# Kernel optimization log

Hardware: AMD Instinct MI355X
Metric: run time of the kernel (lower is better)

Reference implementation:

```python
import jax, jax.numpy as jnp
import numpy as np

S = 8192      # sequence length
D = 768       # bert_out_dim
NA = 256      # num aspects
NO = 256      # num opinions
MAXW = 40     # max span width (width_embedding has 40 entries)
NCAT = 13
NPOL = 3


def setup_inputs() -> dict:
    key = jax.random.key(0)
    ks = jax.random.split(key, 9)
    word_rep = jax.random.normal(ks[0], (S, D), jnp.float32)
    a_head = jax.random.randint(ks[1], (NA,), 0, S - MAXW)
    a_w = jax.random.randint(ks[2], (NA,), 1, MAXW + 1)
    aspects = jnp.stack([a_head, a_head + a_w], axis=-1)  # [NA,2] (head,tail), head<tail
    o_head = jax.random.randint(ks[3], (NO,), 0, S - MAXW)
    o_w = jax.random.randint(ks[4], (NO,), 1, MAXW + 1)
    opinions = jnp.stack([o_head, o_head + o_w], axis=-1)  # [NO,2]
    sc = 0.02
    return {
        'word_rep': word_rep,
        'aspects': aspects,
        'opinions': opinions,
        'W_valid': jax.random.normal(ks[5], (2 * D, 2), jnp.float32) * sc,
        'b_valid': jnp.zeros((2,), jnp.float32),
        'W_cat': jax.random.normal(ks[6], (2 * D, NCAT), jnp.float32) * sc,
        'b_cat': jnp.zeros((NCAT,), jnp.float32),
        'W_pol': jax.random.normal(ks[7], (2 * D, NPOL), jnp.float32) * sc,
        'b_pol': jnp.zeros((NPOL,), jnp.float32),
    }


def _span_maxpool(word_rep, spans):
    # variable-width span max-pool over tokens, vectorized with a gather + mask
    heads, tails = spans[:, 0], spans[:, 1]          # [n]
    pos = heads[:, None] + jnp.arange(MAXW)[None, :]  # [n, MAXW]
    valid = pos < tails[:, None]                      # [n, MAXW]
    g = word_rep[jnp.clip(pos, 0, word_rep.shape[0] - 1)]  # [n, MAXW, D]
    neg = jnp.finfo(word_rep.dtype).min
    return jnp.max(jnp.where(valid[:, :, None], g, neg), axis=1)  # [n, D]


def reference(word_rep, aspects, opinions, W_valid, b_valid, W_cat, b_cat, W_pol, b_pol):
    asp_rep = _span_maxpool(word_rep, aspects)   # [NA, D]
    opi_rep = _span_maxpool(word_rep, opinions)  # [NO, D]
    na, no = asp_rep.shape[0], opi_rep.shape[0]
    # all aspect x opinion pairs (itertools.product order): asp varies slowest
    pair_reps = jnp.concatenate([
        jnp.repeat(asp_rep, no, axis=0),          # [NA*NO, D]
        jnp.tile(opi_rep, (na, 1)),               # [NA*NO, D]
    ], axis=-1)                                    # [NA*NO, 2D]
    asp_ids = jnp.repeat(jnp.arange(na), no)
    opi_ids = jnp.tile(jnp.arange(no), na)

    valid_out = pair_reps @ W_valid + b_valid      # [P, 2]
    cate_out = pair_reps @ W_cat + b_cat           # [P, NCAT]
    polar_out = pair_reps @ W_pol + b_pol          # [P, NPOL]

    valid_mask = valid_out[:, 0] > valid_out[:, 1]  # [P] bool
    # jit-safe masking instead of data-dependent boolean select
    m = valid_mask[:, None]
    return (jnp.where(m, pair_reps, 0.0),
            jnp.where(valid_mask, asp_ids, -1),
            jnp.where(valid_mask, opi_ids, -1),
            jnp.where(m, cate_out, 0.0),
            jnp.where(m, polar_out, 0.0),
            valid_mask)
```

## Files before the change

### kernel.cpp

```cpp
#include <hip/hip_runtime.h>
#include <math.h>

#define S 8192
#define D 768
#define NA 256
#define NO 256
#define MAXW 40
#define NCAT 13
#define NPOL 3
#define NPROJ (2 + NCAT + NPOL)

__global__ __launch_bounds__(256) void span_pool_proj(
    const float* __restrict__ word_rep,
    const int*   __restrict__ aspects,
    const int*   __restrict__ opinions,
    const float* __restrict__ W_valid,
    const float* __restrict__ W_cat,
    const float* __restrict__ W_pol,
    float*  __restrict__ rep_out,
    double* __restrict__ proj_out)
{
    __shared__ float rep[D];
    const int b = blockIdx.x;
    const int t = threadIdx.x;

    const int* spans = (b < NA) ? aspects : opinions;
    const int  s     = (b < NA) ? b : (b - NA);
    const int  woff  = (b < NA) ? 0 : D;

    const int head  = spans[2 * s];
    const int tail  = spans[2 * s + 1];
    const int width = tail - head;

    float m0 = -3.402823466e+38f, m1 = m0, m2 = m0;
    const float* base = word_rep + (size_t)head * D;
    for (int r = 0; r < width; ++r) {
        const float* row = base + (size_t)r * D;
        m0 = fmaxf(m0, row[t]);
        m1 = fmaxf(m1, row[t + 256]);
        m2 = fmaxf(m2, row[t + 512]);
    }
    rep[t] = m0; rep[t + 256] = m1; rep[t + 512] = m2;
    float* orow = rep_out + (size_t)b * D;
    orow[t] = m0; orow[t + 256] = m1; orow[t + 512] = m2;
    __syncthreads();

    if (t < NPROJ) {
        const float* W; int ncol, col;
        if (t < 2)           { W = W_valid; ncol = 2;    col = t; }
        else if (t < 2+NCAT) { W = W_cat;   ncol = NCAT; col = t - 2; }
        else                 { W = W_pol;   ncol = NPOL; col = t - 2 - NCAT; }
        double acc = 0.0;
        for (int d = 0; d < D; ++d)
            acc += (double)rep[d] * (double)W[(size_t)(woff + d) * ncol + col];
        proj_out[(size_t)b * NPROJ + t] = acc;
    }
}

__global__ __launch_bounds__(384) void pair_write(
    const float4* __restrict__ rep4,
    const double* __restrict__ proj,
    const float*  __restrict__ b_valid,
    const float*  __restrict__ b_cat,
    const float*  __restrict__ b_pol,
    float* __restrict__ out)
{
    const int p = blockIdx.x;
    const int i = p >> 8;
    const int j = p & 255;
    const int t = threadIdx.x;

    __shared__ int smask;
    const double* pa = proj + (size_t)i * NPROJ;
    const double* po = proj + (size_t)(NA + j) * NPROJ;

    if (t == 0) {
        double v0 = pa[0] + po[0] + (double)b_valid[0];
        double v1 = pa[1] + po[1] + (double)b_valid[1];
        smask = (v0 > v1) ? 1 : 0;
    }
    __syncthreads();
    const int mask = smask;

    float4 val;
    if (mask) {
        val = (t < 192) ? rep4[(size_t)i * 192 + t]
                        : rep4[(size_t)(NA + j) * 192 + (t - 192)];
    } else {
        val = make_float4(0.f, 0.f, 0.f, 0.f);
    }
    ((float4*)out)[(size_t)p * 384 + t] = val;

    const size_t OFF1 = (size_t)NA * NO * 2 * D;
    const size_t OFF2 = OFF1 + (size_t)NA * NO;
    const size_t OFF3 = OFF2 + (size_t)NA * NO;
    const size_t OFF4 = OFF3 + (size_t)NA * NO * NCAT;
    const size_t OFF5 = OFF4 + (size_t)NA * NO * NPOL;

    if (t == 0) {
        out[OFF1 + p] = mask ? (float)i : -1.0f;
        out[OFF2 + p] = mask ? (float)j : -1.0f;
        out[OFF5 + p] = mask ? 1.0f : 0.0f;
    } else if (t >= 64 && t < 64 + NCAT) {
        const int c = t - 64;
        float v = mask ? (float)(pa[2 + c] + po[2 + c] + (double)b_cat[c]) : 0.0f;
        out[OFF3 + (size_t)p * NCAT + c] = v;
    } else if (t >= 128 && t < 128 + NPOL) {
        const int c = t - 128;
        float v = mask ? (float)(pa[2 + NCAT + c] + po[2 + NCAT + c] + (double)b_pol[c]) : 0.0f;
        out[OFF4 + (size_t)p * NPOL + c] = v;
    }
}

extern "C" void kernel_launch(void* const* d_in, const int* in_sizes, int n_in,
                              void* d_out, int out_size, void* d_ws, size_t ws_size,
                              hipStream_t stream)
{
    const float* word_rep = (const float*)d_in[0];
    const int*   aspects  = (const int*)  d_in[1];
    const int*   opinions = (const int*)  d_in[2];
    const float* W_valid  = (const float*)d_in[3];
    const float* b_valid  = (const float*)d_in[4];
    const float* W_cat    = (const float*)d_in[5];
    const float* b_cat    = (const float*)d_in[6];
    const float* W_pol    = (const float*)d_in[7];
    const float* b_pol    = (const float*)d_in[8];
    float* out = (float*)d_out;

    float*  rep  = (float*)d_ws;
    double* proj = (double*)((char*)d_ws + (size_t)(NA + NO) * D * sizeof(float));

    span_pool_proj<<<NA + NO, 256, 0, stream>>>(
        word_rep, aspects, opinions, W_valid, W_cat, W_pol, rep, proj);

    pair_write<<<NA * NO, 384, 0, stream>>>(
        (const float4*)rep, proj, b_valid, b_cat, b_pol, out);
}
```

Measured before the change: 508.6 us.

## Split pair writer into small-output and streaming kernels with nontemporal stores

Moves the per-pair mask and small outputs (ids, category, polarity, mask) into a separate kernel with one thread per pair and coalesced strided writes, and records a mask buffer. The large pair_reps write becomes a lean streaming kernel that reads the mask and writes with nontemporal stores, without shared memory or a block barrier. It also vectorizes the span max-pool with float4 loads and splits the projection dot product into two accumulators. This adds a third kernel launch and a workspace mask round-trip.

```diff
diff --git a/kernel.cpp b/kernel.cpp
--- a/kernel.cpp
+++ b/kernel.cpp
@@ -9,6 +9,14 @@
 #define NCAT 13
 #define NPOL 3
 #define NPROJ (2 + NCAT + NPOL)
+
+#define OFF1 ((size_t)NA * NO * 2 * D)
+#define OFF2 (OFF1 + (size_t)NA * NO)
+#define OFF3 (OFF2 + (size_t)NA * NO)
+#define OFF4 (OFF3 + (size_t)NA * NO * NCAT)
+#define OFF5 (OFF4 + (size_t)NA * NO * NPOL)
+
+typedef float vfloat4 __attribute__((ext_vector_type(4)));
 
 __global__ __launch_bounds__(256) void span_pool_proj(
     const float* __restrict__ word_rep,
@@ -32,84 +40,84 @@
     const int tail  = spans[2 * s + 1];
     const int width = tail - head;
 
-    float m0 = -3.402823466e+38f, m1 = m0, m2 = m0;
-    const float* base = word_rep + (size_t)head * D;
-    for (int r = 0; r < width; ++r) {
-        const float* row = base + (size_t)r * D;
-        m0 = fmaxf(m0, row[t]);
-        m1 = fmaxf(m1, row[t + 256]);
-        m2 = fmaxf(m2, row[t + 512]);
+    if (t < 192) {
+        const vfloat4* base = (const vfloat4*)(word_rep + (size_t)head * D) + t;
+        vfloat4 m = base[0];
+        for (int r = 1; r < width; ++r) {
+            vfloat4 v = base[(size_t)r * (D / 4)];
+            m.x = fmaxf(m.x, v.x); m.y = fmaxf(m.y, v.y);
+            m.z = fmaxf(m.z, v.z); m.w = fmaxf(m.w, v.w);
+        }
+        ((vfloat4*)rep)[t] = m;
+        ((vfloat4*)(rep_out + (size_t)b * D))[t] = m;
     }
-    rep[t] = m0; rep[t + 256] = m1; rep[t + 512] = m2;
-    float* orow = rep_out + (size_t)b * D;
-    orow[t] = m0; orow[t + 256] = m1; orow[t + 512] = m2;
     __syncthreads();
 
     if (t < NPROJ) {
         const float* W; int ncol, col;
-        if (t < 2)           { W = W_valid; ncol = 2;    col = t; }
-        else if (t < 2+NCAT) { W = W_cat;   ncol = NCAT; col = t - 2; }
-        else                 { W = W_pol;   ncol = NPOL; col = t - 2 - NCAT; }
-        double acc = 0.0;
-        for (int d = 0; d < D; ++d)
-            acc += (double)rep[d] * (double)W[(size_t)(woff + d) * ncol + col];
-        proj_out[(size_t)b * NPROJ + t] = acc;
+        if (t < 2)             { W = W_valid; ncol = 2;    col = t; }
+        else if (t < 2 + NCAT) { W = W_cat;   ncol = NCAT; col = t - 2; }
+        else                   { W = W_pol;   ncol = NPOL; col = t - 2 - NCAT; }
+        double a0 = 0.0, a1 = 0.0;
+        for (int d = 0; d < D; d += 2) {
+            a0 += (double)rep[d]     * (double)W[(size_t)(woff + d)     * ncol + col];
+            a1 += (double)rep[d + 1] * (double)W[(size_t)(woff + d + 1) * ncol + col];
+        }
+        proj_out[(size_t)b * NPROJ + t] = a0 + a1;
     }
 }
 
-__global__ __launch_bounds__(384) void pair_write(
-    const float4* __restrict__ rep4,
+__global__ __launch_bounds__(256) void pair_small(
     const double* __restrict__ proj,
     const float*  __restrict__ b_valid,
     const float*  __restrict__ b_cat,
     const float*  __restrict__ b_pol,
-    float* __restrict__ out)
+    float*    __restrict__ out,
+    unsigned* __restrict__ maskbuf)
 {
-    const int p = blockIdx.x;
-    const int i = p >> 8;
-    const int j = p & 255;
-    const int t = threadIdx.x;
+    const int i = blockIdx.x;
+    const int j = threadIdx.x;
+    const int p = (i << 8) | j;
 
-    __shared__ int smask;
     const double* pa = proj + (size_t)i * NPROJ;
     const double* po = proj + (size_t)(NA + j) * NPROJ;
 
-    if (t == 0) {
-        double v0 = pa[0] + po[0] + (double)b_valid[0];
-        double v1 = pa[1] + po[1] + (double)b_valid[1];
-        smask = (v0 > v1) ? 1 : 0;
-    }
-    __syncthreads();
-    const int mask = smask;
+    const double v0 = pa[0] + po[0] + (double)b_valid[0];
+    const double v1 = pa[1] + po[1] + (double)b_valid[1];
+    const int mask = (v0 > v1) ? 1 : 0;
 
-    float4 val;
-    if (mask) {
-        val = (t < 192) ? rep4[(size_t)i * 192 + t]
-                        : rep4[(size_t)(NA + j) * 192 + (t - 192)];
-    } else {
-        val = make_float4(0.f, 0.f, 0.f, 0.f);
-    }
-    ((float4*)out)[(size_t)p * 384 + t] = val;
-
-    const size_t OFF1 = (size_t)NA * NO * 2 * D;
-    const size_t OFF2 = OFF1 + (size_t)NA * NO;
-    const size_t OFF3 = OFF2 + (size_t)NA * NO;
-    const size_t OFF4 = OFF3 + (size_t)NA * NO * NCAT;
-    const size_t OFF5 = OFF4 + (size_t)NA * NO * NPOL;
-
-    if (t == 0) {
-        out[OFF1 + p] = mask ? (float)i : -1.0f;
-        out[OFF2 + p] = mask ? (float)j : -1.0f;
-        out[OFF5 + p] = mask ? 1.0f : 0.0f;
-    } else if (t >= 64 && t < 64 + NCAT) {
-        const int c = t - 64;
+    maskbuf[p] = (unsigned)mask;
+    out[OFF1 + p] = mask ? (float)i : -1.0f;
+    out[OFF2 + p] = mask ? (float)j : -1.0f;
+    out[OFF5 + p] = mask ? 1.0f : 0.0f;
+#pragma unroll
+    for (int c = 0; c < NCAT; ++c) {
         float v = mask ? (float)(pa[2 + c] + po[2 + c] + (double)b_cat[c]) : 0.0f;
         out[OFF3 + (size_t)p * NCAT + c] = v;
-    } else if (t >= 128 && t < 128 + NPOL) {
-        const int c = t - 128;
+    }
+#pragma unroll
+    for (int c = 0; c < NPOL; ++c) {
         float v = mask ? (float)(pa[2 + NCAT + c] + po[2 + NCAT + c] + (double)b_pol[c]) : 0.0f;
         out[OFF4 + (size_t)p * NPOL + c] = v;
     }
+}
+
+__global__ __launch_bounds__(384) void pair_stream(
+    const vfloat4*  __restrict__ rep4,
+    const unsigned* __restrict__ maskbuf,
+    vfloat4*        __restrict__ out4)
+{
+    const int p = blockIdx.x;
+    const int t = threadIdx.x;
+    const int i = p >> 8;
+    const int j = p & 255;
+
+    vfloat4 val = (vfloat4)0.f;
+    if (maskbuf[p]) {
+        val = (t < 192) ? rep4[(size_t)i * 192 + t]
+                        : rep4[(size_t)(NA + j) * 192 + (t - 192)];
+    }
+    __builtin_nontemporal_store(val, &out4[(size_t)p * 384 + t]);
 }
 
 extern "C" void kernel_launch(void* const* d_in, const int* in_sizes, int n_in,
@@ -127,12 +135,14 @@
     const float* b_pol    = (const float*)d_in[8];
     float* out = (float*)d_out;
 
-    float*  rep  = (float*)d_ws;
-    double* proj = (double*)((char*)d_ws + (size_t)(NA + NO) * D * sizeof(float));
+    float*    rep  = (float*)d_ws;
+    double*   proj = (double*)((char*)d_ws + (size_t)(NA + NO) * D * sizeof(float));
+    unsigned* mask = (unsigned*)((char*)proj + (size_t)(NA + NO) * NPROJ * sizeof(double));
 
     span_pool_proj<<<NA + NO, 256, 0, stream>>>(
         word_rep, aspects, opinions, W_valid, W_cat, W_pol, rep, proj);
 
-    pair_write<<<NA * NO, 384, 0, stream>>>(
-        (const float4*)rep, proj, b_valid, b_cat, b_pol, out);
+    pair_small<<<NA, NO, 0, stream>>>(proj, b_valid, b_cat, b_pol, out, mask);
+
+    pair_stream<<<NA * NO, 384, 0, stream>>>((const vfloat4*)rep, mask, (vfloat4*)out);
 }
```

Result: faster. 476.6 us (-6.3%).
